# Kernel optimization log

Hardware: AMD Instinct MI355X
Metric: run time of the kernel (lower is better)

## Reference

```python
import jax, jax.numpy as jnp
import numpy as np

N = 16384      # nodes (256 chess boards x 64 squares)
E = 393216     # edges (avg degree 24)
G = 256        # graphs
HID = 128
H = 4
C = 32         # head dim
L = 8          # 4 blocks x 2 GATv2Conv
NODE_DIM = 21
EDGE_DIM = 6


def setup_inputs() -> dict:
    key = jax.random.key(0)
    ks = jax.random.split(key, 12)
    x = jax.random.normal(ks[0], (N, NODE_DIM), jnp.float32)
    edge_index = jax.random.randint(ks[1], (2, E), 0, N, dtype=jnp.int32)
    edge_attr = jax.random.uniform(ks[2], (E, EDGE_DIM), dtype=jnp.float32)
    batch = jnp.sort(jax.random.randint(ks[3], (N,), 0, G, dtype=jnp.int32))

    def w(k, shape, fan_in):
        return jax.random.normal(k, shape, jnp.float32) * (1.0 / np.sqrt(fan_in))

    Win = w(ks[4], (NODE_DIM, HID), NODE_DIM)
    b_in = jnp.zeros((HID,), jnp.float32)
    Wl = w(ks[5], (L, HID, HID), HID)
    bl = jnp.zeros((L, HID), jnp.float32)
    Wr = w(ks[6], (L, HID, HID), HID)
    br = jnp.zeros((L, HID), jnp.float32)
    We = w(ks[7], (L, EDGE_DIM, HID), EDGE_DIM)
    att = w(ks[8], (L, H, C), C)
    bconv = jnp.zeros((L, HID), jnp.float32)
    gamma = jnp.ones((L, HID), jnp.float32)
    beta = jnp.zeros((L, HID), jnp.float32)
    W1 = w(ks[9], (HID, 64), HID)
    b1 = jnp.zeros((64,), jnp.float32)
    W2 = w(ks[10], (64, 3), 64)
    b2 = jnp.zeros((3,), jnp.float32)
    return dict(x=x, edge_index=edge_index, edge_attr=edge_attr, batch=batch,
                Win=Win, b_in=b_in, Wl=Wl, bl=bl, Wr=Wr, br=br, We=We, att=att,
                bconv=bconv, gamma=gamma, beta=beta, W1=W1, b1=b1, W2=W2, b2=b2)


def _gatv2(h, src, dst, ea, Wl, bl, Wr, br, We, att, bias):
    # PyG GATv2Conv: message j->i uses x_j from lin_l, x_i from lin_r
    xl = (h @ Wl + bl).reshape(N, H, C)
    xr = (h @ Wr + br).reshape(N, H, C)
    ee = (ea @ We).reshape(-1, H, C)
    m = jax.nn.leaky_relu(xl[src] + xr[dst] + ee, 0.2)   # [Ef, H, C]
    s = jnp.einsum('ehc,hc->eh', m, att)                 # [Ef, H]
    smax = jax.ops.segment_max(s, dst, num_segments=N)   # self-loops => no empty segs
    ex = jnp.exp(s - smax[dst])
    den = jax.ops.segment_sum(ex, dst, num_segments=N)
    alpha = ex / den[dst]                                # edge softmax per target node
    out = jax.ops.segment_sum(alpha[:, :, None] * xl[src], dst, num_segments=N)
    return out.reshape(N, HID) + bias


def _bn(x, g, b):
    mu = jnp.mean(x, axis=0)
    var = jnp.var(x, axis=0)
    return g * (x - mu) * jax.lax.rsqrt(var + 1e-5) + b


def reference(x, edge_index, edge_attr, batch, Win, b_in, Wl, bl, Wr, br, We, att,
              bconv, gamma, beta, W1, b1, W2, b2):
    src0, dst0 = edge_index[0], edge_index[1]
    # add self-loops with fill_value='mean' (per-target mean of incoming edge_attr)
    deg = jax.ops.segment_sum(jnp.ones((E,), jnp.float32), dst0, num_segments=N)
    loop_attr = jax.ops.segment_sum(edge_attr, dst0, num_segments=N) / jnp.maximum(deg, 1.0)[:, None]
    idx = jnp.arange(N, dtype=src0.dtype)
    src = jnp.concatenate([src0, idx])
    dst = jnp.concatenate([dst0, idx])
    ea = jnp.concatenate([edge_attr, loop_attr], axis=0)

    h = jax.nn.relu(x @ Win + b_in)
    for blk in range(4):
        res = h
        l = 2 * blk
        h = jax.nn.relu(_bn(_gatv2(h, src, dst, ea, Wl[l], bl[l], Wr[l], br[l], We[l], att[l], bconv[l]), gamma[l], beta[l]))
        l = 2 * blk + 1
        h = _bn(_gatv2(h, src, dst, ea, Wl[l], bl[l], Wr[l], br[l], We[l], att[l], bconv[l]), gamma[l], beta[l])
        h = jax.nn.relu(h + res)

    cnt = jnp.maximum(jax.ops.segment_sum(jnp.ones((N,), jnp.float32), batch, num_segments=G), 1.0)
    pooled = jax.ops.segment_sum(h, batch, num_segments=G) / cnt[:, None]
    logits = jax.nn.relu(pooled @ W1 + b1) @ W2 + b2
    return logits
```

## Files before the change

### kernel.cpp

```cpp
#include <hip/hip_runtime.h>
#include <math.h>

constexpr int N   = 16384;
constexpr int E   = 393216;
constexpr int EF  = E + N;
constexpr int G   = 256;
constexpr int HID = 128;

__device__ __forceinline__ float red16(float x) {
    union fi { float f; int i; };
    fi a, b;
    a.f = x;
    b.i = __builtin_amdgcn_mov_dpp(a.i, 0x121, 0xf, 0xf, false); a.f += b.f;
    b.i = __builtin_amdgcn_mov_dpp(a.i, 0x122, 0xf, 0xf, false); a.f += b.f;
    b.i = __builtin_amdgcn_mov_dpp(a.i, 0x124, 0xf, 0xf, false); a.f += b.f;
    b.i = __builtin_amdgcn_mov_dpp(a.i, 0x128, 0xf, 0xf, false); a.f += b.f;
    return a.f;
}

__global__ __launch_bounds__(256) void k_hist(const int* __restrict__ dst,
                                              int* __restrict__ cnt) {
    int e = blockIdx.x * 256 + threadIdx.x;
    if (e < E) atomicAdd(&cnt[dst[e]], 1);
}

__global__ __launch_bounds__(1024) void k_scan(const int* __restrict__ cnt,
                                               int* __restrict__ row_ptr) {
    __shared__ int lds[1024];
    int t = threadIdx.x;
    int local[16];
    int s = 0;
    int base = t * 16;
#pragma unroll
    for (int q = 0; q < 16; q++) { local[q] = cnt[base + q] + 1; s += local[q]; }
    lds[t] = s;
    __syncthreads();
    for (int off = 1; off < 1024; off <<= 1) {
        int v = (t >= off) ? lds[t - off] : 0;
        __syncthreads();
        lds[t] += v;
        __syncthreads();
    }
    int run = (t == 0) ? 0 : lds[t - 1];
    if (t == 0) row_ptr[0] = 0;
#pragma unroll
    for (int q = 0; q < 16; q++) { run += local[q]; row_ptr[base + q + 1] = run; }
}

__global__ __launch_bounds__(256) void k_scatter(const int* __restrict__ src,
                                                 const int* __restrict__ dst,
                                                 const int* __restrict__ row_ptr,
                                                 int* __restrict__ fill,
                                                 int* __restrict__ csr_src,
                                                 int* __restrict__ csr_eid) {
    int e = blockIdx.x * 256 + threadIdx.x;
    if (e >= E) return;
    int d = dst[e];
    int pos = row_ptr[d] + atomicAdd(&fill[d], 1);
    csr_src[pos] = src[e];
    csr_eid[pos] = e;
}

__global__ __launch_bounds__(256) void k_selfloop(const int* __restrict__ row_ptr,
                                                  int* __restrict__ csr_src,
                                                  int* __restrict__ csr_eid) {
    int i = blockIdx.x * 256 + threadIdx.x;
    if (i >= N) return;
    int pos = row_ptr[i + 1] - 1;
    csr_src[pos] = i;
    csr_eid[pos] = E + i;
}

__global__ __launch_bounds__(256) void k_build_ea(const int* __restrict__ csr_eid,
                                                  const float* __restrict__ edge_attr,
                                                  float* __restrict__ csr_ea) {
    int p = blockIdx.x * 256 + threadIdx.x;
    if (p >= EF) return;
    int eid = csr_eid[p];
    if (eid >= E) return;
    const float* s = edge_attr + (size_t)eid * 6;
    float4 a = {s[0], s[1], s[2], s[3]};
    float4 b = {s[4], s[5], 0.0f, 0.0f};
    float4* dst = (float4*)(csr_ea + (size_t)p * 8);
    dst[0] = a;
    dst[1] = b;
}

__global__ __launch_bounds__(256) void k_loopattr2(const int* __restrict__ row_ptr,
                                                   float* __restrict__ csr_ea) {
    int i = blockIdx.x * 256 + threadIdx.x;
    if (i >= N) return;
    int e0 = row_ptr[i], e1 = row_ptr[i + 1] - 1;
    float4 sa = {0, 0, 0, 0};
    float sbx = 0.0f, sby = 0.0f;
    for (int e = e0; e < e1; e++) {
        const float4* p = (const float4*)(csr_ea + (size_t)e * 8);
        float4 a = p[0];
        float4 b = p[1];
        sa.x += a.x; sa.y += a.y; sa.z += a.z; sa.w += a.w;
        sbx += b.x; sby += b.y;
    }
    float inv = 1.0f / fmaxf((float)(e1 - e0), 1.0f);
    float4 oa = {sa.x * inv, sa.y * inv, sa.z * inv, sa.w * inv};
    float4 ob = {sbx * inv, sby * inv, 0.0f, 0.0f};
    float4* q = (float4*)(csr_ea + (size_t)e1 * 8);
    q[0] = oa;
    q[1] = ob;
}

__global__ __launch_bounds__(128) void k_ingemm(const float* __restrict__ x,
                                                const float* __restrict__ Win,
                                                const float* __restrict__ b_in,
                                                float* __restrict__ h) {
    __shared__ float xs[21];
    int i = blockIdx.x;
    int c = threadIdx.x;
    if (c < 21) xs[c] = x[i * 21 + c];
    __syncthreads();
    float acc = b_in[c];
#pragma unroll
    for (int d = 0; d < 21; d++) acc += xs[d] * Win[d * HID + c];
    h[i * HID + c] = fmaxf(acc, 0.0f);
}

__global__ __launch_bounds__(256) void k_gemm_lr(const float* __restrict__ h,
                                                 const float* __restrict__ bns,
                                                 const float* __restrict__ gamma,
                                                 const float* __restrict__ beta,
                                                 const float* __restrict__ Wl,
                                                 const float* __restrict__ bl,
                                                 const float* __restrict__ Wr,
                                                 const float* __restrict__ br,
                                                 float* __restrict__ XL,
                                                 float* __restrict__ XR) {
    __shared__ float hs[16][HID];
    __shared__ float sc[HID], sh[HID];
    int t = threadIdx.x;
    int r0 = blockIdx.x * 16;
    if (bns) {
        if (t < 128) {
            const float invN = 1.0f / (float)N;
            float mean = bns[t] * invN;
            float var  = bns[128 + t] * invN - mean * mean;
            float inv  = rsqrtf(var + 1e-5f);
            float s = gamma[t] * inv;
            sc[t] = s;
            sh[t] = beta[t] - mean * s;
        }
        __syncthreads();
    }
    {
        int row = t >> 4;
        int col = (t & 15) * 8;
        const float4* src = (const float4*)&h[(size_t)(r0 + row) * HID + col];
        float4 a = src[0];
        float4 b = src[1];
        if (bns) {
            float4 s0 = *(const float4*)&sc[col];
            float4 s1 = *(const float4*)&sc[col + 4];
            float4 h0 = *(const float4*)&sh[col];
            float4 h1 = *(const float4*)&sh[col + 4];
            a.x = fmaxf(fmaf(a.x, s0.x, h0.x), 0.0f);
            a.y = fmaxf(fmaf(a.y, s0.y, h0.y), 0.0f);
            a.z = fmaxf(fmaf(a.z, s0.z, h0.z), 0.0f);
            a.w = fmaxf(fmaf(a.w, s0.w, h0.w), 0.0f);
            b.x = fmaxf(fmaf(b.x, s1.x, h1.x), 0.0f);
            b.y = fmaxf(fmaf(b.y, s1.y, h1.y), 0.0f);
            b.z = fmaxf(fmaf(b.z, s1.z, h1.z), 0.0f);
            b.w = fmaxf(fmaf(b.w, s1.w, h1.w), 0.0f);
        }
        float4* dst = (float4*)&hs[row][col];
        dst[0] = a;
        dst[1] = b;
    }
    __syncthreads();
    bool right = t >= 128;
    int cp = (t & 63) * 2;
    int rbase = ((t >> 6) & 1) * 8;
    const float* W    = right ? Wr : Wl;
    const float* bias = right ? br : bl;
    float* OUT        = right ? XR : XL;
    float b0 = bias[cp], b1 = bias[cp + 1];
    float acc0[8], acc1[8];
#pragma unroll
    for (int r = 0; r < 8; r++) { acc0[r] = b0; acc1[r] = b1; }
    for (int k = 0; k < HID; k += 4) {
        float4 h4[8];
#pragma unroll
        for (int r = 0; r < 8; r++) h4[r] = *(const float4*)&hs[rbase + r][k];
#pragma unroll
        for (int kk = 0; kk < 4; kk++) {
            float2 w = *(const float2*)&W[(size_t)(k + kk) * HID + cp];
#pragma unroll
            for (int r = 0; r < 8; r++) {
                float hv = ((const float*)&h4[r])[kk];
                acc0[r] = fmaf(hv, w.x, acc0[r]);
                acc1[r] = fmaf(hv, w.y, acc1[r]);
            }
        }
    }
#pragma unroll
    for (int r = 0; r < 8; r++) {
        float2 o = {acc0[r], acc1[r]};
        *(float2*)&OUT[(size_t)(r0 + rbase + r) * HID + cp] = o;
    }
}

__device__ __forceinline__ void pf_xl(int e, int e1,
                                      const int* __restrict__ csr_src,
                                      const float* __restrict__ xl, int ch0,
                                      float2 out[4]) {
#pragma unroll
    for (int k = 0; k < 4; k++) {
        int ec = (e + k < e1) ? e + k : e1 - 1;
        int j = __builtin_amdgcn_readfirstlane(csr_src[ec]);
        out[k] = *(const float2*)&xl[(size_t)j * HID + ch0];
    }
}

__global__ __launch_bounds__(256) void k_edge(const int* __restrict__ row_ptr,
                                              const int* __restrict__ csr_src,
                                              const float* __restrict__ csr_ea,
                                              const float* __restrict__ xl,
                                              const float* __restrict__ xr,
                                              const float* __restrict__ We_l,
                                              const float* __restrict__ att_l,
                                              float* __restrict__ gout) {
    int wave = (blockIdx.x * blockDim.x + threadIdx.x) >> 6;
    int lane = threadIdx.x & 63;
    if (wave >= N) return;
    int i = wave;
    int hh = lane >> 4;
    int ss = lane & 15;
    int ch0 = hh * 32 + 2 * ss;

    float2 xr2 = *(const float2*)&xr[(size_t)i * HID + ch0];
    float a0 = att_l[ch0], a1 = att_l[ch0 + 1];
    float we0[6], we1[6];
#pragma unroll
    for (int d = 0; d < 6; d++) {
        float2 w = *(const float2*)&We_l[d * HID + ch0];
        we0[d] = w.x;
        we1[d] = w.y;
    }

    float rm = -INFINITY, rd = 0.0f, acc0 = 0.0f, acc1 = 0.0f;

    int e0 = __builtin_amdgcn_readfirstlane(row_ptr[i]);
    int e1 = __builtin_amdgcn_readfirstlane(row_ptr[i + 1]);

    auto body = [&](int e, const float2 xlv[4]) {
        float p[4];
#pragma unroll
        for (int k = 0; k < 4; k++) {
            int ee = e + k;
            int ec = (ee < e1) ? ee : (e1 - 1);
            const float4* ea4 = (const float4*)(csr_ea + (size_t)ec * 8);
            float4 eaA = ea4[0];
            float4 eaB = ea4[1];
            float s0 = eaA.x * we0[0], s1 = eaA.x * we1[0];
            s0 = fmaf(eaA.y, we0[1], s0); s1 = fmaf(eaA.y, we1[1], s1);
            s0 = fmaf(eaA.z, we0[2], s0); s1 = fmaf(eaA.z, we1[2], s1);
            s0 = fmaf(eaA.w, we0[3], s0); s1 = fmaf(eaA.w, we1[3], s1);
            s0 = fmaf(eaB.x, we0[4], s0); s1 = fmaf(eaB.x, we1[4], s1);
            s0 = fmaf(eaB.y, we0[5], s0); s1 = fmaf(eaB.y, we1[5], s1);
            float m0 = xlv[k].x + xr2.x + s0;
            float m1 = xlv[k].y + xr2.y + s1;
            m0 = fmaxf(m0, 0.2f * m0);
            m1 = fmaxf(m1, 0.2f * m1);
            float pv = m0 * a0;
            pv = fmaf(m1, a1, pv);
            pv = red16(pv);
            p[k] = (ee < e1) ? pv : -INFINITY;
        }
        float bm = fmaxf(fmaxf(p[0], p[1]), fmaxf(p[2], p[3]));
        float nm = fmaxf(rm, bm);
        float sc = __expf(rm - nm);
        rd *= sc; acc0 *= sc; acc1 *= sc;
#pragma unroll
        for (int k = 0; k < 4; k++) {
            float ek = __expf(p[k] - nm);
            rd += ek;
            acc0 = fmaf(ek, xlv[k].x, acc0);
            acc1 = fmaf(ek, xlv[k].y, acc1);
        }
        rm = nm;
    };

    float2 bufA[4], bufB[4];
    pf_xl(e0, e1, csr_src, xl, ch0, bufA);
    for (int e = e0; e < e1; e += 8) {
        pf_xl(e + 4, e1, csr_src, xl, ch0, bufB);
        body(e, bufA);
        pf_xl(e + 8, e1, csr_src, xl, ch0, bufA);
        if (e + 4 < e1) body(e + 4, bufB);
    }
    float inv = 1.0f / rd;
    float2 o = {acc0 * inv, acc1 * inv};
    *(float2*)&gout[(size_t)i * HID + ch0] = o;
}

__global__ __launch_bounds__(256) void k_bnstats(const float* __restrict__ v,
                                                 float* __restrict__ sums) {
    __shared__ float l_s[256], l_q[256];
    int t = threadIdx.x;
    int c = t & 127;
    int half = t >> 7;
    int r = blockIdx.x * 64 + half;
    float s = 0.0f, q = 0.0f;
    for (int it = 0; it < 32; it++, r += 2) {
        float val = v[(size_t)r * HID + c];
        s += val;
        q += val * val;
    }
    l_s[t] = s; l_q[t] = q;
    __syncthreads();
    if (t < 128) {
        s = l_s[t] + l_s[t + 128];
        q = l_q[t] + l_q[t + 128];
        atomicAdd(&sums[c], s);
        atomicAdd(&sums[128 + c], q);
    }
}

__global__ __launch_bounds__(256) void k_bnapply(const float* __restrict__ g,
                                                 const float* __restrict__ sums,
                                                 const float* __restrict__ gamma,
                                                 const float* __restrict__ beta,
                                                 const float* __restrict__ res,
                                                 float* __restrict__ out) {
    int idx4 = (blockIdx.x * 256 + threadIdx.x) * 4;
    int c = idx4 & 127;
    const float invN = 1.0f / (float)N;
    float4 gv = *(const float4*)&g[idx4];
    float4 s4 = *(const float4*)&sums[c];
    float4 q4 = *(const float4*)&sums[128 + c];
    float4 gm = *(const float4*)&gamma[c];
    float4 bt = *(const float4*)&beta[c];
    float4 o;
    {
        float mean = s4.x * invN, var = q4.x * invN - mean * mean;
        o.x = gm.x * (gv.x - mean) * rsqrtf(var + 1e-5f) + bt.x;
        mean = s4.y * invN; var = q4.y * invN - mean * mean;
        o.y = gm.y * (gv.y - mean) * rsqrtf(var + 1e-5f) + bt.y;
        mean = s4.z * invN; var = q4.z * invN - mean * mean;
        o.z = gm.z * (gv.z - mean) * rsqrtf(var + 1e-5f) + bt.z;
        mean = s4.w * invN; var = q4.w * invN - mean * mean;
        o.w = gm.w * (gv.w - mean) * rsqrtf(var + 1e-5f) + bt.w;
    }
    float4 r4 = *(const float4*)&res[idx4];
    o.x = fmaxf(o.x + r4.x, 0.0f);
    o.y = fmaxf(o.y + r4.y, 0.0f);
    o.z = fmaxf(o.z + r4.z, 0.0f);
    o.w = fmaxf(o.w + r4.w, 0.0f);
    *(float4*)&out[idx4] = o;
}

__global__ __launch_bounds__(128) void k_pool(const float* __restrict__ h,
                                              const int* __restrict__ batch,
                                              const float* __restrict__ W1,
                                              const float* __restrict__ b1,
                                              const float* __restrict__ W2,
                                              const float* __restrict__ b2,
                                              float* __restrict__ out) {
    __shared__ float pooled[HID];
    __shared__ float hid[64];
    __shared__ int bounds[2];
    int g = blockIdx.x;
    int t = threadIdx.x;
    if (t < 2) {
        int target = g + t;
        int lo = 0, hi = N;
        while (lo < hi) {
            int mid = (lo + hi) >> 1;
            if (batch[mid] < target) lo = mid + 1; else hi = mid;
        }
        bounds[t] = lo;
    }
    __syncthreads();
    int s = bounds[0], e = bounds[1];
    float acc = 0.0f;
    for (int r = s; r < e; r++) acc += h[(size_t)r * HID + t];
    float cntf = fmaxf((float)(e - s), 1.0f);
    pooled[t] = acc / cntf;
    __syncthreads();
    if (t < 64) {
        float a = b1[t];
#pragma unroll 4
        for (int c = 0; c < HID; c++) a += pooled[c] * W1[c * 64 + t];
        hid[t] = fmaxf(a, 0.0f);
    }
    __syncthreads();
    if (t < 3) {
        float a = b2[t];
#pragma unroll
        for (int j = 0; j < 64; j++) a += hid[j] * W2[j * 3 + t];
        out[g * 3 + t] = a;
    }
}

extern "C" void kernel_launch(void* const* d_in, const int* in_sizes, int n_in,
                              void* d_out, int out_size, void* d_ws, size_t ws_size,
                              hipStream_t stream) {
    const float* x         = (const float*)d_in[0];
    const int*   edge_index= (const int*)d_in[1];
    const float* edge_attr = (const float*)d_in[2];
    const int*   batch     = (const int*)d_in[3];
    const float* Win       = (const float*)d_in[4];
    const float* b_in      = (const float*)d_in[5];
    const float* Wl        = (const float*)d_in[6];
    const float* bl        = (const float*)d_in[7];
    const float* Wr        = (const float*)d_in[8];
    const float* br        = (const float*)d_in[9];
    const float* We        = (const float*)d_in[10];
    const float* att       = (const float*)d_in[11];
    const float* gamma     = (const float*)d_in[13];
    const float* beta      = (const float*)d_in[14];
    const float* W1        = (const float*)d_in[15];
    const float* b1        = (const float*)d_in[16];
    const float* W2        = (const float*)d_in[17];
    const float* b2        = (const float*)d_in[18];
    float* out = (float*)d_out;

    const int* src0 = edge_index;
    const int* dst0 = edge_index + E;

    char* ws = (char*)d_ws;
    size_t off = 0;
    auto alloc = [&](size_t bytes) -> void* {
        void* p = ws + off;
        off += (bytes + 255) & ~(size_t)255;
        return p;
    };
    int*   cnt       = (int*)alloc((size_t)2 * N * sizeof(int));
    int*   fill      = cnt + N;
    float* bnsums    = (float*)alloc((size_t)8 * 256 * sizeof(float));
    int*   row_ptr   = (int*)alloc((size_t)(N + 1) * sizeof(int));
    int*   csr_src   = (int*)alloc((size_t)EF * sizeof(int));
    int*   csr_eid   = (int*)alloc((size_t)EF * sizeof(int));
    float* csr_ea    = (float*)alloc((size_t)EF * 8 * sizeof(float));
    float* H0        = (float*)alloc((size_t)N * HID * sizeof(float));
    float* XL        = (float*)alloc((size_t)N * HID * sizeof(float));
    float* XR        = (float*)alloc((size_t)N * HID * sizeof(float));
    float* GOUT      = (float*)alloc((size_t)N * HID * sizeof(float));

    size_t zbytes = (size_t)2 * N * sizeof(int) + 8 * 256 * sizeof(float);
    hipMemsetAsync(cnt, 0, zbytes, stream);
    k_hist<<<(E + 255) / 256, 256, 0, stream>>>(dst0, cnt);
    k_scan<<<1, 1024, 0, stream>>>(cnt, row_ptr);
    k_scatter<<<(E + 255) / 256, 256, 0, stream>>>(src0, dst0, row_ptr, fill,
                                                   csr_src, csr_eid);
    k_selfloop<<<(N + 255) / 256, 256, 0, stream>>>(row_ptr, csr_src, csr_eid);
    k_build_ea<<<(EF + 255) / 256, 256, 0, stream>>>(csr_eid, edge_attr, csr_ea);
    k_loopattr2<<<(N + 255) / 256, 256, 0, stream>>>(row_ptr, csr_ea);
    k_ingemm<<<N, 128, 0, stream>>>(x, Win, b_in, H0);

    for (int l = 0; l < 8; l++) {
        bool odd = (l & 1) != 0;
        const float* hin = odd ? GOUT : H0;
        const float* bns_in = odd ? (bnsums + (l - 1) * 256) : nullptr;
        const float* g_in  = odd ? (gamma + (l - 1) * HID) : nullptr;
        const float* b_in2 = odd ? (beta  + (l - 1) * HID) : nullptr;
        k_gemm_lr<<<N / 16, 256, 0, stream>>>(hin, bns_in, g_in, b_in2,
                                              Wl + (size_t)l * HID * HID, bl + l * HID,
                                              Wr + (size_t)l * HID * HID, br + l * HID,
                                              XL, XR);
        k_edge<<<N / 4, 256, 0, stream>>>(row_ptr, csr_src, csr_ea,
                                          XL, XR,
                                          We + (size_t)l * 6 * HID,
                                          att + (size_t)l * HID, GOUT);
        float* bns = bnsums + l * 256;
        k_bnstats<<<256, 256, 0, stream>>>(GOUT, bns);
        if (odd) {
            k_bnapply<<<(N * HID) / 1024, 256, 0, stream>>>(GOUT, bns,
                                                            gamma + l * HID,
                                                            beta + l * HID,
                                                            H0, H0);
        }
    }
    k_pool<<<G, 128, 0, stream>>>(H0, batch, W1, b1, W2, b2, out);
}
```

Measured before the change: 759.3 us.

## Fuse batchnorm stats into edge kernel and BN-apply/residual into next GEMM and pool

After: 875.5 us. 15.3% more time.

```diff
diff --git a/kernel.cpp b/kernel.cpp
--- a/kernel.cpp
+++ b/kernel.cpp
@@ -50,40 +50,37 @@
 __global__ __launch_bounds__(256) void k_scatter(const int* __restrict__ src,
                                                  const int* __restrict__ dst,
                                                  const int* __restrict__ row_ptr,
-                                                 int* __restrict__ fill,
+                                                 int* __restrict__ cnt,
                                                  int* __restrict__ csr_src,
                                                  int* __restrict__ csr_eid) {
     int e = blockIdx.x * 256 + threadIdx.x;
     if (e >= E) return;
     int d = dst[e];
-    int pos = row_ptr[d] + atomicAdd(&fill[d], 1);
+    int pos = row_ptr[d] + atomicSub(&cnt[d], 1) - 1;
     csr_src[pos] = src[e];
     csr_eid[pos] = e;
 }
 
-__global__ __launch_bounds__(256) void k_selfloop(const int* __restrict__ row_ptr,
+__global__ __launch_bounds__(256) void k_build_ea(const int* __restrict__ row_ptr,
                                                   int* __restrict__ csr_src,
-                                                  int* __restrict__ csr_eid) {
-    int i = blockIdx.x * 256 + threadIdx.x;
-    if (i >= N) return;
-    int pos = row_ptr[i + 1] - 1;
-    csr_src[pos] = i;
-    csr_eid[pos] = E + i;
-}
-
-__global__ __launch_bounds__(256) void k_build_ea(const int* __restrict__ csr_eid,
+                                                  int* __restrict__ csr_eid,
                                                   const float* __restrict__ edge_attr,
                                                   float* __restrict__ csr_ea) {
     int p = blockIdx.x * 256 + threadIdx.x;
+    if (p < N) {
+        int pos = row_ptr[p + 1] - 1;
+        csr_src[pos] = p;
+        csr_eid[pos] = E + p;
+    }
     if (p >= EF) return;
-    int eid = csr_eid[p];
-    if (eid >= E) return;
+    unsigned eid = (unsigned)csr_eid[p];
+    if (eid >= (unsigned)E) return;
     const float* s = edge_attr + (size_t)eid * 6;
     float4 a = {s[0], s[1], s[2], s[3]};
     float4 b = {s[4], s[5], 0.0f, 0.0f};
-    float4* dst = (float4*)(csr_ea + (size_t)p * 8);
-    dst[0] = a;
-    dst[1] = b;
+    float4* dstp = (float4*)(csr_ea + (size_t)p * 8);
+    dstp[0] = a;
+    dstp[1] = b;
 }
 
 __global__ __launch_bounds__(256) void k_loopattr2(const int* __restrict__ row_ptr,
@@ -127,6 +124,7 @@
                                                  const float* __restrict__ bns,
                                                  const float* __restrict__ gamma,
                                                  const float* __restrict__ beta,
+                                                 float* __restrict__ res,
                                                  const float* __restrict__ Wl,
                                                  const float* __restrict__ bl,
                                                  const float* __restrict__ Wr,
@@ -152,7 +150,8 @@
     {
         int row = t >> 4;
         int col = (t & 15) * 8;
-        const float4* src = (const float4*)&h[(size_t)(r0 + row) * HID + col];
+        size_t base = (size_t)(r0 + row) * HID + col;
+        const float4* src = (const float4*)&h[base];
         float4 a = src[0];
         float4 b = src[1];
         if (bns) {
@@ -160,14 +159,30 @@
             float4 s1 = *(const float4*)&sc[col + 4];
             float4 h0 = *(const float4*)&sh[col];
             float4 h1 = *(const float4*)&sh[col + 4];
-            a.x = fmaxf(fmaf(a.x, s0.x, h0.x), 0.0f);
-            a.y = fmaxf(fmaf(a.y, s0.y, h0.y), 0.0f);
-            a.z = fmaxf(fmaf(a.z, s0.z, h0.z), 0.0f);
-            a.w = fmaxf(fmaf(a.w, s0.w, h0.w), 0.0f);
-            b.x = fmaxf(fmaf(b.x, s1.x, h1.x), 0.0f);
-            b.y = fmaxf(fmaf(b.y, s1.y, h1.y), 0.0f);
-            b.z = fmaxf(fmaf(b.z, s1.z, h1.z), 0.0f);
-            b.w = fmaxf(fmaf(b.w, s1.w, h1.w), 0.0f);
+            a.x = fmaf(a.x, s0.x, h0.x);
+            a.y = fmaf(a.y, s0.y, h0.y);
+            a.z = fmaf(a.z, s0.z, h0.z);
+            a.w = fmaf(a.w, s0.w, h0.w);
+            b.x = fmaf(b.x, s1.x, h1.x);
+            b.y = fmaf(b.y, s1.y, h1.y);
+            b.z = fmaf(b.z, s1.z, h1.z);
+            b.w = fmaf(b.w, s1.w, h1.w);
+            if (res) {
+                const float4* rp = (const float4*)&res[base];
+                float4 ra = rp[0];
+                float4 rb = rp[1];
+                a.x += ra.x; a.y += ra.y; a.z += ra.z; a.w += ra.w;
+                b.x += rb.x; b.y += rb.y; b.z += rb.z; b.w += rb.w;
+            }
+            a.x = fmaxf(a.x, 0.0f); a.y = fmaxf(a.y, 0.0f);
+            a.z = fmaxf(a.z, 0.0f); a.w = fmaxf(a.w, 0.0f);
+            b.x = fmaxf(b.x, 0.0f); b.y = fmaxf(b.y, 0.0f);
+            b.z = fmaxf(b.z, 0.0f); b.w = fmaxf(b.w, 0.0f);
+            if (res) {
+                float4* wp = (float4*)&res[base];
+                wp[0] = a;
+                wp[1] = b;
+            }
         }
         float4* dst = (float4*)&hs[row][col];
         dst[0] = a;
@@ -225,138 +240,106 @@
                                               const float* __restrict__ xr,
                                               const float* __restrict__ We_l,
                                               const float* __restrict__ att_l,
-                                              float* __restrict__ gout) {
-    int wave = (blockIdx.x * blockDim.x + threadIdx.x) >> 6;
+                                              float* __restrict__ gout,
+                                              float* __restrict__ bnsums) {
+    __shared__ float ls[4][HID], lq[4][HID];
+    int w = threadIdx.x >> 6;
     int lane = threadIdx.x & 63;
-    if (wave >= N) return;
-    int i = wave;
     int hh = lane >> 4;
     int ss = lane & 15;
     int ch0 = hh * 32 + 2 * ss;
 
-    float2 xr2 = *(const float2*)&xr[(size_t)i * HID + ch0];
     float a0 = att_l[ch0], a1 = att_l[ch0 + 1];
     float we0[6], we1[6];
 #pragma unroll
     for (int d = 0; d < 6; d++) {
-        float2 w = *(const float2*)&We_l[d * HID + ch0];
-        we0[d] = w.x;
-        we1[d] = w.y;
-    }
-
-    float rm = -INFINITY, rd = 0.0f, acc0 = 0.0f, acc1 = 0.0f;
-
-    int e0 = __builtin_amdgcn_readfirstlane(row_ptr[i]);
-    int e1 = __builtin_amdgcn_readfirstlane(row_ptr[i + 1]);
-
-    auto body = [&](int e, const float2 xlv[4]) {
-        float p[4];
-#pragma unroll
-        for (int k = 0; k < 4; k++) {
-            int ee = e + k;
-            int ec = (ee < e1) ? ee : (e1 - 1);
-            const float4* ea4 = (const float4*)(csr_ea + (size_t)ec * 8);
-            float4 eaA = ea4[0];
-            float4 eaB = ea4[1];
-            float s0 = eaA.x * we0[0], s1 = eaA.x * we1[0];
-            s0 = fmaf(eaA.y, we0[1], s0); s1 = fmaf(eaA.y, we1[1], s1);
-            s0 = fmaf(eaA.z, we0[2], s0); s1 = fmaf(eaA.z, we1[2], s1);
-            s0 = fmaf(eaA.w, we0[3], s0); s1 = fmaf(eaA.w, we1[3], s1);
-            s0 = fmaf(eaB.x, we0[4], s0); s1 = fmaf(eaB.x, we1[4], s1);
-            s0 = fmaf(eaB.y, we0[5], s0); s1 = fmaf(eaB.y, we1[5], s1);
-            float m0 = xlv[k].x + xr2.x + s0;
-            float m1 = xlv[k].y + xr2.y + s1;
-            m0 = fmaxf(m0, 0.2f * m0);
-            m1 = fmaxf(m1, 0.2f * m1);
-            float pv = m0 * a0;
-            pv = fmaf(m1, a1, pv);
-            pv = red16(pv);
-            p[k] = (ee < e1) ? pv : -INFINITY;
-        }
-        float bm = fmaxf(fmaxf(p[0], p[1]), fmaxf(p[2], p[3]));
-        float nm = fmaxf(rm, bm);
-        float sc = __expf(rm - nm);
-        rd *= sc; acc0 *= sc; acc1 *= sc;
-#pragma unroll
-        for (int k = 0; k < 4; k++) {
-            float ek = __expf(p[k] - nm);
-            rd += ek;
-            acc0 = fmaf(ek, xlv[k].x, acc0);
-            acc1 = fmaf(ek, xlv[k].y, acc1);
-        }
-        rm = nm;
-    };
-
-    float2 bufA[4], bufB[4];
-    pf_xl(e0, e1, csr_src, xl, ch0, bufA);
-    for (int e = e0; e < e1; e += 8) {
-        pf_xl(e + 4, e1, csr_src, xl, ch0, bufB);
-        body(e, bufA);
-        pf_xl(e + 8, e1, csr_src, xl, ch0, bufA);
-        if (e + 4 < e1) body(e + 4, bufB);
-    }
-    float inv = 1.0f / rd;
-    float2 o = {acc0 * inv, acc1 * inv};
-    *(float2*)&gout[(size_t)i * HID + ch0] = o;
-}
-
-__global__ __launch_bounds__(256) void k_bnstats(const float* __restrict__ v,
-                                                 float* __restrict__ sums) {
-    __shared__ float l_s[256], l_q[256];
+        float2 wv = *(const float2*)&We_l[d * HID + ch0];
+        we0[d] = wv.x;
+        we1[d] = wv.y;
+    }
+
+    float s0 = 0.0f, q0 = 0.0f, s1 = 0.0f, q1 = 0.0f;
+    int nbase = blockIdx.x * 16 + w * 4;
+
+    for (int nq = 0; nq < 4; nq++) {
+        int i = nbase + nq;
+        float2 xr2 = *(const float2*)&xr[(size_t)i * HID + ch0];
+        float rm = -INFINITY, rd = 0.0f, acc0 = 0.0f, acc1 = 0.0f;
+        int e0 = __builtin_amdgcn_readfirstlane(row_ptr[i]);
+        int e1 = __builtin_amdgcn_readfirstlane(row_ptr[i + 1]);
+
+        auto body = [&](int e, const float2 xlv[4]) {
+            float p[4];
+#pragma unroll
+            for (int k = 0; k < 4; k++) {
+                int ee = e + k;
+                int ec = (ee < e1) ? ee : (e1 - 1);
+                const float4* ea4 = (const float4*)(csr_ea + (size_t)ec * 8);
+                float4 eaA = ea4[0];
+                float4 eaB = ea4[1];
+                float u0 = eaA.x * we0[0], u1 = eaA.x * we1[0];
+                u0 = fmaf(eaA.y, we0[1], u0); u1 = fmaf(eaA.y, we1[1], u1);
+                u0 = fmaf(eaA.z, we0[2], u0); u1 = fmaf(eaA.z, we1[2], u1);
+                u0 = fmaf(eaA.w, we0[3], u0); u1 = fmaf(eaA.w, we1[3], u1);
+                u0 = fmaf(eaB.x, we0[4], u0); u1 = fmaf(eaB.x, we1[4], u1);
+                u0 = fmaf(eaB.y, we0[5], u0); u1 = fmaf(eaB.y, we1[5], u1);
+                float m0 = xlv[k].x + xr2.x + u0;
+                float m1 = xlv[k].y + xr2.y + u1;
+                m0 = fmaxf(m0, 0.2f * m0);
+                m1 = fmaxf(m1, 0.2f * m1);
+                float pv = m0 * a0;
+                pv = fmaf(m1, a1, pv);
+                pv = red16(pv);
+                p[k] = (ee < e1) ? pv : -INFINITY;
+            }
+            float bm = fmaxf(fmaxf(p[0], p[1]), fmaxf(p[2], p[3]));
+            float nm = fmaxf(rm, bm);
+            float scal = __expf(rm - nm);
+            rd *= scal; acc0 *= scal; acc1 *= scal;
+#pragma unroll
+            for (int k = 0; k < 4; k++) {
+                float ek = __expf(p[k] - nm);
+                rd += ek;
+                acc0 = fmaf(ek, xlv[k].x, acc0);
+                acc1 = fmaf(ek, xlv[k].y, acc1);
+            }
+            rm = nm;
+        };
+
+        float2 bufA[4], bufB[4];
+        pf_xl(e0, e1, csr_src, xl, ch0, bufA);
+        for (int e = e0; e < e1; e += 8) {
+            pf_xl(e + 4, e1, csr_src, xl, ch0, bufB);
+            body(e, bufA);
+            pf_xl(e + 8, e1, csr_src, xl, ch0, bufA);
+            if (e + 4 < e1) body(e + 4, bufB);
+        }
+        float inv = 1.0f / rd;
+        float2 o = {acc0 * inv, acc1 * inv};
+        *(float2*)&gout[(size_t)i * HID + ch0] = o;
+        s0 += o.x; q0 = fmaf(o.x, o.x, q0);
+        s1 += o.y; q1 = fmaf(o.y, o.y, q1);
+    }
+
+    ls[w][ch0] = s0; ls[w][ch0 + 1] = s1;
+    lq[w][ch0] = q0; lq[w][ch0 + 1] = q1;
+    __syncthreads();
     int t = threadIdx.x;
-    int c = t & 127;
-    int half = t >> 7;
-    int r = blockIdx.x * 64 + half;
-    float s = 0.0f, q = 0.0f;
-    for (int it = 0; it < 32; it++, r += 2) {
-        float val = v[(size_t)r * HID + c];
-        s += val;
-        q += val * val;
-    }
-    l_s[t] = s; l_q[t] = q;
-    __syncthreads();
     if (t < 128) {
-        s = l_s[t] + l_s[t + 128];
-        q = l_q[t] + l_q[t + 128];
-        atomicAdd(&sums[c], s);
-        atomicAdd(&sums[128 + c], q);
-    }
-}
-
-__global__ __launch_bounds__(256) void k_bnapply(const float* __restrict__ g,
-                                                 const float* __restrict__ sums,
-                                                 const float* __restrict__ gamma,
-                                                 const float* __restrict__ beta,
-                                                 const float* __restrict__ res,
-                                                 float* __restrict__ out) {
-    int idx4 = (blockIdx.x * 256 + threadIdx.x) * 4;
-    int c = idx4 & 127;
-    const float invN = 1.0f / (float)N;
-    float4 gv = *(const float4*)&g[idx4];
-    float4 s4 = *(const float4*)&sums[c];
-    float4 q4 = *(const float4*)&sums[128 + c];
-    float4 gm = *(const float4*)&gamma[c];
-    float4 bt = *(const float4*)&beta[c];
-    float4 o;
-    {
-        float mean = s4.x * invN, var = q4.x * invN - mean * mean;
-        o.x = gm.x * (gv.x - mean) * rsqrtf(var + 1e-5f) + bt.x;
-        mean = s4.y * invN; var = q4.y * invN - mean * mean;
-        o.y = gm.y * (gv.y - mean) * rsqrtf(var + 1e-5f) + bt.y;
-        mean = s4.z * invN; var = q4.z * invN - mean * mean;
-        o.z = gm.z * (gv.z - mean) * rsqrtf(var + 1e-5f) + bt.z;
-        mean = s4.w * invN; var = q4.w * invN - mean * mean;
-        o.w = gm.w * (gv.w - mean) * rsqrtf(var + 1e-5f) + bt.w;
-    }
-    float4 r4 = *(const float4*)&res[idx4];
-    o.x = fmaxf(o.x + r4.x, 0.0f);
-    o.y = fmaxf(o.y + r4.y, 0.0f);
-    o.z = fmaxf(o.z + r4.z, 0.0f);
-    o.w = fmaxf(o.w + r4.w, 0.0f);
-    *(float4*)&out[idx4] = o;
-}
-
-__global__ __launch_bounds__(128) void k_pool(const float* __restrict__ h,
+        float s = ls[0][t] + ls[1][t] + ls[2][t] + ls[3][t];
+        atomicAdd(&bnsums[t], s);
+    } else {
+        int c = t - 128;
+        float q = lq[0][c] + lq[1][c] + lq[2][c] + lq[3][c];
+        atomicAdd(&bnsums[128 + c], q);
+    }
+}
+
+__global__ __launch_bounds__(128) void k_pool(const float* __restrict__ gout,
+                                              const float* __restrict__ res,
+                                              const float* __restrict__ bns,
+                                              const float* __restrict__ gamma,
+                                              const float* __restrict__ beta,
                                               const int* __restrict__ batch,
                                               const float* __restrict__ W1,
                                               const float* __restrict__ b1,
@@ -377,10 +360,18 @@
         }
         bounds[t] = lo;
     }
+    const float invN = 1.0f / (float)N;
+    float mean = bns[t] * invN;
+    float var  = bns[128 + t] * invN - mean * mean;
+    float scb  = gamma[t] * rsqrtf(var + 1e-5f);
+    float shb  = beta[t] - mean * scb;
     __syncthreads();
     int s = bounds[0], e = bounds[1];
     float acc = 0.0f;
-    for (int r = s; r < e; r++) acc += h[(size_t)r * HID + t];
+    for (int r = s; r < e; r++) {
+        float v = fmaf(gout[(size_t)r * HID + t], scb, shb) + res[(size_t)r * HID + t];
+        acc += fmaxf(v, 0.0f);
+    }
     float cntf = fmaxf((float)(e - s), 1.0f);
     pooled[t] = acc / cntf;
     __syncthreads();
@@ -432,8 +423,7 @@
         off += (bytes + 255) & ~(size_t)255;
         return p;
     };
-    int*   cnt       = (int*)alloc((size_t)2 * N * sizeof(int));
-    int*   fill      = cnt + N;
+    int*   cnt       = (int*)alloc((size_t)N * sizeof(int));
     float* bnsums    = (float*)alloc((size_t)8 * 256 * sizeof(float));
     int*   row_ptr   = (int*)alloc((size_t)(N + 1) * sizeof(int));
     int*   csr_src   = (int*)alloc((size_t)EF * sizeof(int));
@@ -444,39 +434,44 @@
     float* XR        = (float*)alloc((size_t)N * HID * sizeof(float));
     float* GOUT      = (float*)alloc((size_t)N * HID * sizeof(float));
 
-    size_t zbytes = (size_t)2 * N * sizeof(int) + 8 * 256 * sizeof(float);
+    size_t zbytes = (size_t)N * sizeof(int) + 8 * 256 * sizeof(float);
     hipMemsetAsync(cnt, 0, zbytes, stream);
     k_hist<<<(E + 255) / 256, 256, 0, stream>>>(dst0, cnt);
     k_scan<<<1, 1024, 0, stream>>>(cnt, row_ptr);
-    k_scatter<<<(E + 255) / 256, 256, 0, stream>>>(src0, dst0, row_ptr, fill,
+    k_scatter<<<(E + 255) / 256, 256, 0, stream>>>(src0, dst0, row_ptr, cnt,
                                                    csr_src, csr_eid);
-    k_selfloop<<<(N + 255) / 256, 256, 0, stream>>>(row_ptr, csr_src, csr_eid);
-    k_build_ea<<<(EF + 255) / 256, 256, 0, stream>>>(csr_eid, edge_attr, csr_ea);
+    k_build_ea<<<(EF + 255) / 256, 256, 0, stream>>>(row_ptr, csr_src, csr_eid,
+                                                     edge_attr, csr_ea);
     k_loopattr2<<<(N + 255) / 256, 256, 0, stream>>>(row_ptr, csr_ea);
     k_ingemm<<<N, 128, 0, stream>>>(x, Win, b_in, H0);
 
     for (int l = 0; l < 8; l++) {
         bool odd = (l & 1) != 0;
-        const float* hin = odd ? GOUT : H0;
-        const float* bns_in = odd ? (bnsums + (l - 1) * 256) : nullptr;
-        const float* g_in  = odd ? (gamma + (l - 1) * HID) : nullptr;
-        const float* b_in2 = odd ? (beta  + (l - 1) * HID) : nullptr;
-        k_gemm_lr<<<N / 16, 256, 0, stream>>>(hin, bns_in, g_in, b_in2,
+        const float* hin;
+        const float* bns_in = nullptr;
+        const float* g_in = nullptr;
+        const float* b_in2 = nullptr;
+        float* res = nullptr;
+        if (l == 0) {
+            hin = H0;
+        } else {
+            hin = GOUT;
+            bns_in = bnsums + (l - 1) * 256;
+            g_in  = gamma + (size_t)(l - 1) * HID;
+            b_in2 = beta  + (size_t)(l - 1) * HID;
+            if (!odd) res = H0;
+        }
+        k_gemm_lr<<<N / 16, 256, 0, stream>>>(hin, bns_in, g_in, b_in2, res,
                                               Wl + (size_t)l * HID * HID, bl + l * HID,
                                               Wr + (size_t)l * HID * HID, br + l * HID,
                                               XL, XR);
-        k_edge<<<N / 4, 256, 0, stream>>>(row_ptr, csr_src, csr_ea,
-                                          XL, XR,
-                                          We + (size_t)l * 6 * HID,
-                                          att + (size_t)l * HID, GOUT);
-        float* bns = bnsums + l * 256;
-        k_bnstats<<<256, 256, 0, stream>>>(GOUT, bns);
-        if (odd) {
-            k_bnapply<<<(N * HID) / 1024, 256, 0, stream>>>(GOUT, bns,
-                                                            gamma + l * HID,
-                                                            beta + l * HID,
-                                                            H0, H0);
-        }
-    }
-    k_pool<<<G, 128, 0, stream>>>(H0, batch, W1, b1, W2, b2, out);
-}
+        k_edge<<<N / 16, 256, 0, stream>>>(row_ptr, csr_src, csr_ea,
+                                           XL, XR,
+                                           We + (size_t)l * 6 * HID,
+                                           att + (size_t)l * HID, GOUT,
+                                           bnsums + l * 256);
+    }
+    k_pool<<<G, 128, 0, stream>>>(GOUT, H0, bnsums + 7 * 256,
+                                  gamma + 7 * HID, beta + 7 * HID,
+                                  batch, W1, b1, W2, b2, out);
+}
```
